# Performance work log

Hardware: AMD Instinct MI355X
Metric: run time of the kernel (lower is better)

## Reference

```python
import jax, jax.numpy as jnp
import numpy as np

NEG_SLOPE = 0.01  # torch nn.LeakyReLU default


def setup_inputs() -> dict:
    key = jax.random.key(0)
    k1, k2, k3, k4 = jax.random.split(key, 4)
    N, D = 8192, 64
    x = jax.random.normal(k1, (N, D), dtype=jnp.float32)
    W = jax.random.normal(k2, (D, D), dtype=jnp.float32) * (1.0 / np.sqrt(D))
    b = jax.random.normal(k3, (D,), dtype=jnp.float32) * 0.01
    a = jax.random.normal(k4, (2 * D, 1), dtype=jnp.float32)
    return {"x": x, "W": W, "b": b, "a": a}


def reference(x, W, b, a):
    # h = Linear(x): torch stores weight as [out, in], y = x @ W.T + b
    h = x @ W.T + b  # [N, D]
    D = h.shape[1]
    a1 = a[:D, 0]   # weights on the column node (e_x[i,j] = x_j)
    a2 = a[D:, 0]   # weights on the row node    (e_y[i,j] = x_i)
    s1 = h @ a1     # [N], contribution of node j
    s2 = h @ a2     # [N], contribution of node i
    # score[i, j] = a1.h_j + a2.h_i  (equivalent to expand+concat+matmul)
    scores = s2[:, None] + s1[None, :]                       # [N, N]
    scores = jnp.where(scores >= 0, scores, NEG_SLOPE * scores)  # leaky_relu
    att = jax.nn.softmax(scores, axis=1)                     # softmax over j
    # NOTE: forward multiplies attention with the ORIGINAL x, not h
    return att @ x                                           # [N, D]
```

## Files before the change

### kernel.cpp

```cpp
#include <hip/hip_runtime.h>

#define NEG_SLOPE 0.01f

constexpr int N = 8192;
constexpr int D = 64;
constexpr int PB = 32;
constexpr int RB = 32;

typedef __bf16 bf16x8 __attribute__((ext_vector_type(8)));
typedef float f32x4 __attribute__((ext_vector_type(4)));

__global__ __launch_bounds__(256) void gat_prep(
    const float* __restrict__ x, const float* __restrict__ W_,
    const float* __restrict__ b, const float* __restrict__ a,
    float* __restrict__ s1g, float* __restrict__ s2g,
    float* __restrict__ blockmax, bf16x8* __restrict__ xf) {
  __shared__ float w1s[D], w2s[D], cs[2];
  __shared__ float s1loc[PB];

  const int t = threadIdx.x;
  const int bid = blockIdx.x;

  if (t < 128) {
    const int sel = t >> 6, d = t & 63;
    const float* av = a + sel * D;
    float acc = 0.f;
#pragma unroll
    for (int k = 0; k < D; ++k) acc += W_[k * D + d] * av[k];
    (sel ? w2s : w1s)[d] = acc;
  }
  if (t == 128 || t == 129) {
    const int sel = t - 128;
    float acc = 0.f;
    for (int d = 0; d < D; ++d) acc += b[d] * a[sel * D + d];
    cs[sel] = acc;
  }
  __syncthreads();

  {
    const int r = t >> 3, seg = t & 7;
    const int gi = bid * PB + r;
    const float4 xa = *(const float4*)(x + (size_t)gi * D + seg * 8);
    const float4 xb = *(const float4*)(x + (size_t)gi * D + seg * 8 + 4);
    float p1 = xa.x * w1s[seg * 8 + 0] + xa.y * w1s[seg * 8 + 1] +
               xa.z * w1s[seg * 8 + 2] + xa.w * w1s[seg * 8 + 3] +
               xb.x * w1s[seg * 8 + 4] + xb.y * w1s[seg * 8 + 5] +
               xb.z * w1s[seg * 8 + 6] + xb.w * w1s[seg * 8 + 7];
    float p2 = xa.x * w2s[seg * 8 + 0] + xa.y * w2s[seg * 8 + 1] +
               xa.z * w2s[seg * 8 + 2] + xa.w * w2s[seg * 8 + 3] +
               xb.x * w2s[seg * 8 + 4] + xb.y * w2s[seg * 8 + 5] +
               xb.z * w2s[seg * 8 + 6] + xb.w * w2s[seg * 8 + 7];
#pragma unroll
    for (int off = 4; off; off >>= 1) {
      p1 += __shfl_xor(p1, off, 64);
      p2 += __shfl_xor(p2, off, 64);
    }
    if (seg == 0) {
      const float v1 = p1 + cs[0], v2 = p2 + cs[1];
      s1g[gi] = v1;
      s2g[gi] = v2;
      s1loc[r] = v1;
    }
  }

  {
    const int dt = t >> 6, fl = t & 63;
    const int jb = bid * PB + ((fl >> 4) << 3);
    const int col = dt * 16 + (fl & 15);
    bf16x8 f;
#pragma unroll
    for (int q = 0; q < 8; ++q) f[q] = (__bf16)x[(size_t)(jb + q) * D + col];
    xf[(bid << 8) | (dt << 6) | fl] = f;
  }
  __syncthreads();
  if (t == 0) {
    float m = s1loc[0];
#pragma unroll
    for (int r = 1; r < PB; ++r) m = fmaxf(m, s1loc[r]);
    blockmax[bid] = m;
  }
}

__global__ __launch_bounds__(256, 2) void gat_main(
    const bf16x8* __restrict__ xf, const float* __restrict__ s1g,
    const float* __restrict__ s2g, const float* __restrict__ blockmax,
    float* __restrict__ out) {
  __shared__ float accT[4][RB][64];
  __shared__ float zt[4][RB];
  __shared__ float gms;

  const int t = threadIdx.x;
  const int lane = t & 63;
  const int w = t >> 6;
  const int arow = lane & 15;
  const int grp = lane >> 4;
  const int ibase = blockIdx.x * RB;

  if (w == 0) {
    float v = fmaxf(fmaxf(blockmax[lane], blockmax[lane + 64]),
                    fmaxf(blockmax[lane + 128], blockmax[lane + 192]));
#pragma unroll
    for (int off = 32; off; off >>= 1) v = fmaxf(v, __shfl_xor(v, off, 64));
    if (lane == 0) gms = v;
  }
  __syncthreads();
  const float gm = gms;

  const float s2v0 = s2g[ibase + arow];
  const float s2v1 = s2g[ibase + 16 + arow];
  const float tm0 = s2v0 + gm, tm1 = s2v1 + gm;
  const float mneg0 = -fmaxf(tm0, NEG_SLOPE * tm0);
  const float mneg1 = -fmaxf(tm1, NEG_SLOPE * tm1);

  f32x4 a00 = {0.f, 0.f, 0.f, 0.f}, a01 = a00, a02 = a00, a03 = a00;
  f32x4 a10 = a00, a11 = a00, a12 = a00, a13 = a00;
  float zz0 = 0.f, zz1 = 0.f;

  int c = w;
  bf16x8 xb0 = xf[(c << 8) + 0 * 64 + lane];
  bf16x8 xb1 = xf[(c << 8) + 1 * 64 + lane];
  bf16x8 xb2 = xf[(c << 8) + 2 * 64 + lane];
  bf16x8 xb3 = xf[(c << 8) + 3 * 64 + lane];
  float4 sa = *(const float4*)(s1g + c * 32 + grp * 8);
  float4 sb = *(const float4*)(s1g + c * 32 + grp * 8 + 4);

  for (int i = 0; i < N / 32 / 4; ++i) {
    const int cn = (i == N / 32 / 4 - 1) ? c : c + 4;
    bf16x8 nb0 = xf[(cn << 8) + 0 * 64 + lane];
    bf16x8 nb1 = xf[(cn << 8) + 1 * 64 + lane];
    bf16x8 nb2 = xf[(cn << 8) + 2 * 64 + lane];
    bf16x8 nb3 = xf[(cn << 8) + 3 * 64 + lane];
    const float4 na = *(const float4*)(s1g + cn * 32 + grp * 8);
    const float4 nbb = *(const float4*)(s1g + cn * 32 + grp * 8 + 4);

    bf16x8 pa0, pa1;
    {
      const float* sv = &sa.x;
#pragma unroll
      for (int q = 0; q < 4; ++q) {
        const float t0 = s2v0 + sv[q];
        const float p0 = __expf(fmaxf(t0, NEG_SLOPE * t0) + mneg0);
        zz0 += p0;
        pa0[q] = (__bf16)p0;
        const float t1 = s2v1 + sv[q];
        const float p1 = __expf(fmaxf(t1, NEG_SLOPE * t1) + mneg1);
        zz1 += p1;
        pa1[q] = (__bf16)p1;
      }
      const float* sw = &sb.x;
#pragma unroll
      for (int q = 0; q < 4; ++q) {
        const float t0 = s2v0 + sw[q];
        const float p0 = __expf(fmaxf(t0, NEG_SLOPE * t0) + mneg0);
        zz0 += p0;
        pa0[4 + q] = (__bf16)p0;
        const float t1 = s2v1 + sw[q];
        const float p1 = __expf(fmaxf(t1, NEG_SLOPE * t1) + mneg1);
        zz1 += p1;
        pa1[4 + q] = (__bf16)p1;
      }
    }

    a00 = __builtin_amdgcn_mfma_f32_16x16x32_bf16(pa0, xb0, a00, 0, 0, 0);
    a01 = __builtin_amdgcn_mfma_f32_16x16x32_bf16(pa0, xb1, a01, 0, 0, 0);
    a02 = __builtin_amdgcn_mfma_f32_16x16x32_bf16(pa0, xb2, a02, 0, 0, 0);
    a03 = __builtin_amdgcn_mfma_f32_16x16x32_bf16(pa0, xb3, a03, 0, 0, 0);
    a10 = __builtin_amdgcn_mfma_f32_16x16x32_bf16(pa1, xb0, a10, 0, 0, 0);
    a11 = __builtin_amdgcn_mfma_f32_16x16x32_bf16(pa1, xb1, a11, 0, 0, 0);
    a12 = __builtin_amdgcn_mfma_f32_16x16x32_bf16(pa1, xb2, a12, 0, 0, 0);
    a13 = __builtin_amdgcn_mfma_f32_16x16x32_bf16(pa1, xb3, a13, 0, 0, 0);

    xb0 = nb0; xb1 = nb1; xb2 = nb2; xb3 = nb3;
    sa = na; sb = nbb;
    c += 4;
  }

  zz0 += __shfl_xor(zz0, 16, 64);
  zz0 += __shfl_xor(zz0, 32, 64);
  zz1 += __shfl_xor(zz1, 16, 64);
  zz1 += __shfl_xor(zz1, 32, 64);
  if (lane < 16) {
    zt[w][arow] = zz0;
    zt[w][16 + arow] = zz1;
  }

#pragma unroll
  for (int reg = 0; reg < 4; ++reg) {
    accT[w][grp * 4 + reg][0 * 16 + arow] = a00[reg];
    accT[w][grp * 4 + reg][1 * 16 + arow] = a01[reg];
    accT[w][grp * 4 + reg][2 * 16 + arow] = a02[reg];
    accT[w][grp * 4 + reg][3 * 16 + arow] = a03[reg];
    accT[w][16 + grp * 4 + reg][0 * 16 + arow] = a10[reg];
    accT[w][16 + grp * 4 + reg][1 * 16 + arow] = a11[reg];
    accT[w][16 + grp * 4 + reg][2 * 16 + arow] = a12[reg];
    accT[w][16 + grp * 4 + reg][3 * 16 + arow] = a13[reg];
  }
  __syncthreads();

#pragma unroll
  for (int k = 0; k < 8; ++k) {
    const int r = w * 8 + k;
    const float s = accT[0][r][lane] + accT[1][r][lane] + accT[2][r][lane] + accT[3][r][lane];
    const float z = zt[0][r] + zt[1][r] + zt[2][r] + zt[3][r];
    out[(size_t)(ibase + r) * D + lane] = s / z;
  }
}

extern "C" void kernel_launch(void* const* d_in, const int* in_sizes, int n_in,
                              void* d_out, int out_size, void* d_ws, size_t ws_size,
                              hipStream_t stream) {
  const float* x = (const float*)d_in[0];
  const float* W = (const float*)d_in[1];
  const float* b = (const float*)d_in[2];
  const float* a = (const float*)d_in[3];

  float* s1 = (float*)d_ws;
  float* s2 = s1 + N;
  float* blockmax = s2 + N;
  bf16x8* xf = (bf16x8*)((char*)d_ws + (1u << 20));
  float* out = (float*)d_out;

  gat_prep<<<N / PB, 256, 0, stream>>>(x, W, b, a, s1, s2, blockmax, xf);
  gat_main<<<N / RB, 256, 0, stream>>>(xf, s1, s2, blockmax, out);
}
```

Before: 88.90 us.

## Use 8 waves per block, exp2 with prescaled scores, MFMA row sums

Doubles the number of waves per block in the main kernel (512 threads, 8 waves each taking every 8th key chunk), so per-wave loop length halves and latency hiding improves, at the cost of a larger LDS reduction buffer. Folds log2(e) into the projected attention weights in the prep kernel so the inner loop can use a raw exp2 instead of __expf. Computes the softmax denominators with an extra MFMA against a ones vector instead of scalar adds and shuffles. The MFMA sum now uses the bf16-rounded probabilities, which matches the numerator's rounding but slightly changes numerics.

```diff
diff --git a/kernel.cpp b/kernel.cpp
--- a/kernel.cpp
+++ b/kernel.cpp
@@ -1,14 +1,22 @@
 #include <hip/hip_runtime.h>
 
 #define NEG_SLOPE 0.01f
+#define LOG2E 1.4426950408889634f
 
 constexpr int N = 8192;
 constexpr int D = 64;
 constexpr int PB = 32;
 constexpr int RB = 32;
+constexpr int NW = 8;
 
 typedef __bf16 bf16x8 __attribute__((ext_vector_type(8)));
 typedef float f32x4 __attribute__((ext_vector_type(4)));
+
+#if __has_builtin(__builtin_amdgcn_exp2f)
+#define EXP2(x) __builtin_amdgcn_exp2f(x)
+#else
+#define EXP2(x) exp2f(x)
+#endif
 
 __global__ __launch_bounds__(256) void gat_prep(
     const float* __restrict__ x, const float* __restrict__ W_,
@@ -27,13 +35,13 @@
     float acc = 0.f;
 #pragma unroll
     for (int k = 0; k < D; ++k) acc += W_[k * D + d] * av[k];
-    (sel ? w2s : w1s)[d] = acc;
+    (sel ? w2s : w1s)[d] = acc * LOG2E;
   }
   if (t == 128 || t == 129) {
     const int sel = t - 128;
     float acc = 0.f;
     for (int d = 0; d < D; ++d) acc += b[d] * a[sel * D + d];
-    cs[sel] = acc;
+    cs[sel] = acc * LOG2E;
   }
   __syncthreads();
 
@@ -81,12 +89,12 @@
   }
 }
 
-__global__ __launch_bounds__(256, 2) void gat_main(
+__global__ __launch_bounds__(512, 2) void gat_main(
     const bf16x8* __restrict__ xf, const float* __restrict__ s1g,
     const float* __restrict__ s2g, const float* __restrict__ blockmax,
     float* __restrict__ out) {
-  __shared__ float accT[4][RB][64];
-  __shared__ float zt[4][RB];
+  __shared__ float accT[NW][RB][64];
+  __shared__ float zt[NW][RB];
   __shared__ float gms;
 
   const int t = threadIdx.x;
@@ -96,7 +104,7 @@
   const int grp = lane >> 4;
   const int ibase = blockIdx.x * RB;
 
-  if (w == 0) {
+  if (t < 64) {
     float v = fmaxf(fmaxf(blockmax[lane], blockmax[lane + 64]),
                     fmaxf(blockmax[lane + 128], blockmax[lane + 192]));
 #pragma unroll
@@ -114,7 +122,10 @@
 
   f32x4 a00 = {0.f, 0.f, 0.f, 0.f}, a01 = a00, a02 = a00, a03 = a00;
   f32x4 a10 = a00, a11 = a00, a12 = a00, a13 = a00;
-  float zz0 = 0.f, zz1 = 0.f;
+  f32x4 az0 = a00, az1 = a00;
+  bf16x8 ones;
+#pragma unroll
+  for (int q = 0; q < 8; ++q) ones[q] = (__bf16)1.0f;
 
   int c = w;
   bf16x8 xb0 = xf[(c << 8) + 0 * 64 + lane];
@@ -124,8 +135,9 @@
   float4 sa = *(const float4*)(s1g + c * 32 + grp * 8);
   float4 sb = *(const float4*)(s1g + c * 32 + grp * 8 + 4);
 
-  for (int i = 0; i < N / 32 / 4; ++i) {
-    const int cn = (i == N / 32 / 4 - 1) ? c : c + 4;
+  constexpr int ITERS = N / 32 / NW;
+  for (int i = 0; i < ITERS; ++i) {
+    const int cn = (i == ITERS - 1) ? c : c + NW;
     bf16x8 nb0 = xf[(cn << 8) + 0 * 64 + lane];
     bf16x8 nb1 = xf[(cn << 8) + 1 * 64 + lane];
     bf16x8 nb2 = xf[(cn << 8) + 2 * 64 + lane];
@@ -139,25 +151,17 @@
 #pragma unroll
       for (int q = 0; q < 4; ++q) {
         const float t0 = s2v0 + sv[q];
-        const float p0 = __expf(fmaxf(t0, NEG_SLOPE * t0) + mneg0);
-        zz0 += p0;
-        pa0[q] = (__bf16)p0;
+        pa0[q] = (__bf16)EXP2(fmaxf(t0, NEG_SLOPE * t0) + mneg0);
         const float t1 = s2v1 + sv[q];
-        const float p1 = __expf(fmaxf(t1, NEG_SLOPE * t1) + mneg1);
-        zz1 += p1;
-        pa1[q] = (__bf16)p1;
+        pa1[q] = (__bf16)EXP2(fmaxf(t1, NEG_SLOPE * t1) + mneg1);
       }
       const float* sw = &sb.x;
 #pragma unroll
       for (int q = 0; q < 4; ++q) {
         const float t0 = s2v0 + sw[q];
-        const float p0 = __expf(fmaxf(t0, NEG_SLOPE * t0) + mneg0);
-        zz0 += p0;
-        pa0[4 + q] = (__bf16)p0;
+        pa0[4 + q] = (__bf16)EXP2(fmaxf(t0, NEG_SLOPE * t0) + mneg0);
         const float t1 = s2v1 + sw[q];
-        const float p1 = __expf(fmaxf(t1, NEG_SLOPE * t1) + mneg1);
-        zz1 += p1;
-        pa1[4 + q] = (__bf16)p1;
+        pa1[4 + q] = (__bf16)EXP2(fmaxf(t1, NEG_SLOPE * t1) + mneg1);
       }
     }
 
@@ -165,23 +169,24 @@
     a01 = __builtin_amdgcn_mfma_f32_16x16x32_bf16(pa0, xb1, a01, 0, 0, 0);
     a02 = __builtin_amdgcn_mfma_f32_16x16x32_bf16(pa0, xb2, a02, 0, 0, 0);
     a03 = __builtin_amdgcn_mfma_f32_16x16x32_bf16(pa0, xb3, a03, 0, 0, 0);
+    az0 = __builtin_amdgcn_mfma_f32_16x16x32_bf16(pa0, ones, az0, 0, 0, 0);
     a10 = __builtin_amdgcn_mfma_f32_16x16x32_bf16(pa1, xb0, a10, 0, 0, 0);
     a11 = __builtin_amdgcn_mfma_f32_16x16x32_bf16(pa1, xb1, a11, 0, 0, 0);
     a12 = __builtin_amdgcn_mfma_f32_16x16x32_bf16(pa1, xb2, a12, 0, 0, 0);
     a13 = __builtin_amdgcn_mfma_f32_16x16x32_bf16(pa1, xb3, a13, 0, 0, 0);
+    az1 = __builtin_amdgcn_mfma_f32_16x16x32_bf16(pa1, ones, az1, 0, 0, 0);
 
     xb0 = nb0; xb1 = nb1; xb2 = nb2; xb3 = nb3;
     sa = na; sb = nbb;
-    c += 4;
-  }
-
-  zz0 += __shfl_xor(zz0, 16, 64);
-  zz0 += __shfl_xor(zz0, 32, 64);
-  zz1 += __shfl_xor(zz1, 16, 64);
-  zz1 += __shfl_xor(zz1, 32, 64);
-  if (lane < 16) {
-    zt[w][arow] = zz0;
-    zt[w][16 + arow] = zz1;
+    c += NW;
+  }
+
+  if (arow == 0) {
+#pragma unroll
+    for (int reg = 0; reg < 4; ++reg) {
+      zt[w][grp * 4 + reg] = az0[reg];
+      zt[w][16 + grp * 4 + reg] = az1[reg];
+    }
   }
 
 #pragma unroll
@@ -198,10 +203,14 @@
   __syncthreads();
 
 #pragma unroll
-  for (int k = 0; k < 8; ++k) {
-    const int r = w * 8 + k;
-    const float s = accT[0][r][lane] + accT[1][r][lane] + accT[2][r][lane] + accT[3][r][lane];
-    const float z = zt[0][r] + zt[1][r] + zt[2][r] + zt[3][r];
+  for (int k = 0; k < 4; ++k) {
+    const int r = w * 4 + k;
+    float s = 0.f, z = 0.f;
+#pragma unroll
+    for (int v = 0; v < NW; ++v) {
+      s += accT[v][r][lane];
+      z += zt[v][r];
+    }
     out[(size_t)(ibase + r) * D + lane] = s / z;
   }
 }
@@ -221,5 +230,5 @@
   float* out = (float*)d_out;
 
   gat_prep<<<N / PB, 256, 0, stream>>>(x, W, b, a, s1, s2, blockmax, xf);
-  gat_main<<<N / RB, 256, 0, stream>>>(xf, s1, s2, blockmax, out);
+  gat_main<<<N / RB, 512, 0, stream>>>(xf, s1, s2, blockmax, out);
 }
```

Result: slower. 91.60 us (+3.0%).
